# Kernel tuning notes

Measured on AMD Instinct MI355X. Metric: run time of the kernel, lower is better.

The kernel has to match this reference:

```python
import jax, jax.numpy as jnp
import numpy as np

B, H, W = 8, 48, 48
D_MODEL, D_STATE, SSM_RATIO, K = 192, 16, 2.0, 4
D_INNER = int(SSM_RATIO * D_MODEL)        # 384
DT_RANK = int(np.ceil(D_MODEL / 16))       # 12
EPS = 1e-6


def setup_inputs() -> dict:
    key = jax.random.key(0)
    ks = jax.random.split(key, 12)
    s = 0.02
    inp = {
        "x": jax.random.normal(ks[0], (B, H, W, D_MODEL), jnp.float32),
        "in_proj_w": s * jax.random.normal(ks[1], (2 * D_INNER, D_MODEL), jnp.float32),
        "conv_w": s * jax.random.normal(ks[2], (D_INNER, 1, 3, 3), jnp.float32),
        "conv_b": jnp.zeros((D_INNER,), jnp.float32),
        "x_proj_w": s * jax.random.normal(ks[3], (K, DT_RANK + 2 * D_STATE, D_INNER), jnp.float32),
        "dt_w": s * jax.random.normal(ks[4], (K, D_INNER, DT_RANK), jnp.float32),
        "dt_bias": 0.05 * jax.random.normal(ks[5], (K, D_INNER), jnp.float32),
        "A_logs": jnp.log(jnp.broadcast_to(jnp.arange(1, D_STATE + 1, dtype=jnp.float32), (K * D_INNER, D_STATE)).copy()),
        "Ds": jnp.ones((K * D_INNER,), jnp.float32),
        "ln_w": jnp.ones((D_INNER,), jnp.float32),
        "ln_b": jnp.zeros((D_INNER,), jnp.float32),
        "out_proj_w": s * jax.random.normal(ks[6], (D_MODEL, D_INNER), jnp.float32),
    }
    return inp


def _selective_scan(u, dt, A, Bs, Cs):
    # u, dt: (B,K,D,L); A: (K,D,N); Bs, Cs: (B,K,N,L)
    u_t = jnp.moveaxis(u, -1, 0)    # (L,B,K,D)
    dt_t = jnp.moveaxis(dt, -1, 0)  # (L,B,K,D)
    B_t = jnp.moveaxis(Bs, -1, 0)   # (L,B,K,N)
    C_t = jnp.moveaxis(Cs, -1, 0)   # (L,B,K,N)
    b = u.shape[0]
    h0 = jnp.zeros((b, K, D_INNER, D_STATE), jnp.float32)

    def step(h, inp):
        ut, dtt, bt, ct = inp
        dA = jnp.exp(dtt[..., None] * A)                       # (B,K,D,N)
        h = dA * h + (dtt * ut)[..., None] * bt[:, :, None, :]  # (B,K,D,N)
        y = jnp.einsum('bkdn,bkn->bkd', h, ct)
        return h, y

    _, ys = jax.lax.scan(step, h0, (u_t, dt_t, B_t, C_t))
    return jnp.moveaxis(ys, 0, -1)  # (B,K,D,L)


def reference(x, in_proj_w, conv_w, conv_b, x_proj_w, dt_w, dt_bias, A_logs, Ds, ln_w, ln_b, out_proj_w):
    b, h, w, _ = x.shape
    L = h * w
    # in_proj + split into x / gate z
    xz = jnp.einsum('bhwc,oc->bhwo', x, in_proj_w)
    xi, z = jnp.split(xz, 2, axis=-1)
    z = jax.nn.silu(z)
    # depthwise 3x3 conv, channel-first
    xi = jnp.transpose(xi, (0, 3, 1, 2))  # (B,Di,H,W)
    xi = jax.lax.conv_general_dilated(
        xi, conv_w, window_strides=(1, 1), padding='SAME',
        feature_group_count=D_INNER,
        dimension_numbers=('NCHW', 'OIHW', 'NCHW')) + conv_b[None, :, None, None]
    xi = jax.nn.silu(xi)
    # cross-scan: 4 directions (row-major, col-major, and their reverses)
    xr = xi.reshape(b, D_INNER, L)
    xc = jnp.transpose(xi, (0, 1, 3, 2)).reshape(b, D_INNER, L)
    xs = jnp.stack([xr, xc, jnp.flip(xr, -1), jnp.flip(xc, -1)], axis=1)  # (B,K,D,L)
    # per-direction projections
    x_dbl = jnp.einsum('bkdl,kcd->bkcl', xs, x_proj_w)  # (B,K,R+2N,L)
    dts = x_dbl[:, :, :DT_RANK]
    Bs = x_dbl[:, :, DT_RANK:DT_RANK + D_STATE]
    Cs = x_dbl[:, :, DT_RANK + D_STATE:]
    dts = jnp.einsum('bkrl,kdr->bkdl', dts, dt_w)
    A = -jnp.exp(A_logs.astype(jnp.float32)).reshape(K, D_INNER, D_STATE)
    dt = jax.nn.softplus(dts + dt_bias[None, :, :, None])
    ys = _selective_scan(xs.astype(jnp.float32), dt, A, Bs.astype(jnp.float32), Cs.astype(jnp.float32))
    ys = ys + Ds.reshape(1, K, D_INNER, 1) * xs  # skip
    # cross-merge (invert each direction, sum)
    def col2row(t):
        return jnp.transpose(t.reshape(b, D_INNER, w, h), (0, 1, 3, 2)).reshape(b, D_INNER, L)
    y = ys[:, 0] + col2row(ys[:, 1]) + jnp.flip(ys[:, 2], -1) + col2row(jnp.flip(ys[:, 3], -1))
    y = jnp.transpose(y.reshape(b, D_INNER, h, w), (0, 2, 3, 1))  # (B,H,W,Di)
    # LayerNorm over channel dim
    mu = y.mean(-1, keepdims=True)
    var = ((y - mu) ** 2).mean(-1, keepdims=True)
    y = (y - mu) / jnp.sqrt(var + EPS) * ln_w + ln_b
    # gate + out_proj
    y = y * z
    out = jnp.einsum('bhwd,od->bhwo', y, out_proj_w)
    return out.astype(x.dtype)
```

## Files before the change

kernel.cpp:

```cpp
#include <hip/hip_runtime.h>

#define BB 8
#define HH 48
#define WW2 48
#define LL 2304
#define CIN 192
#define DI 384
#define NK 4
#define RR 12
#define NS 16
#define CD 44
#define NX 176
#define MM 18432
#define NC 32
#define CL 72

typedef unsigned short u16;
typedef __attribute__((ext_vector_type(8))) short s16x8;
typedef __attribute__((ext_vector_type(4))) float f32x4;

static __device__ __forceinline__ float siluf(float x) { return x / (1.f + __expf(-x)); }

static __device__ __forceinline__ u16 f2bf(float x) {
    unsigned u = __float_as_uint(x);
    return (u16)((u + 0x7FFFu + ((u >> 16) & 1u)) >> 16);
}
static __device__ __forceinline__ float bf2f(u16 h) {
    return __uint_as_float(((unsigned)h) << 16);
}

static __device__ __forceinline__ int posmap(int k, int l) {
    switch (k & 3) {
    case 0: return l;
    case 1: { int w = l / HH; int h = l - w * HH; return h * WW2 + w; }
    case 2: return LL - 1 - l;
    default: { int j = LL - 1 - l; int w = j / HH; int h = j - w * HH; return h * WW2 + w; }
    }
}

__global__ __launch_bounds__(256) void k_cvt2(const float* __restrict__ in,
                                              u16* __restrict__ hi,
                                              u16* __restrict__ lo, int n) {
    int i = (blockIdx.x * 256 + threadIdx.x) * 4;
    if (i >= n) return;
    float4 v = *(const float4*)(in + i);
    u16 h0 = f2bf(v.x), h1 = f2bf(v.y), h2 = f2bf(v.z), h3 = f2bf(v.w);
    hi[i + 0] = h0; hi[i + 1] = h1; hi[i + 2] = h2; hi[i + 3] = h3;
    lo[i + 0] = f2bf(v.x - bf2f(h0));
    lo[i + 1] = f2bf(v.y - bf2f(h1));
    lo[i + 2] = f2bf(v.z - bf2f(h2));
    lo[i + 3] = f2bf(v.w - bf2f(h3));
}

template<int N, int K, int EPI>
__global__ __launch_bounds__(256) void k_gemm(const u16* __restrict__ Ahg,
                                              const u16* __restrict__ Alg,
                                              const u16* __restrict__ Bhg,
                                              const u16* __restrict__ Blg,
                                              float* __restrict__ O1,
                                              float* __restrict__ O2) {
    __shared__ __align__(16) u16 lds[12288];
    const int m0 = blockIdx.x << 7;
    const int n0 = blockIdx.y << 6;
    const int t = threadIdx.x;
    const int lane = t & 63;
    const int w = t >> 6;
    const int wm = w & 1, wn = w >> 1;

    f32x4 acc[4][2];
#pragma unroll
    for (int mi = 0; mi < 4; ++mi)
#pragma unroll
        for (int ni = 0; ni < 2; ++ni)
#pragma unroll
            for (int r = 0; r < 4; ++r) acc[mi][ni][r] = 0.f;

    const int rA = lane & 15;
    const int kb = (lane >> 4) << 3;

    for (int k0 = 0; k0 < K; k0 += 32) {
#pragma unroll
        for (int rep = 0; rep < 2; ++rep) {
            int q = t + (rep << 8);
            int row = q >> 2;
            int kk = (q & 3) << 3;
            size_t ga = (size_t)(m0 + row) * K + k0 + kk;
            *(uint4*)&lds[(row << 5) + kk] = *(const uint4*)(Ahg + ga);
            *(uint4*)&lds[4096 + (row << 5) + kk] = *(const uint4*)(Alg + ga);
        }
        {
            int row = t >> 2;
            int kk = (t & 3) << 3;
            int rg = n0 + row;
            if (N & 63) rg = (rg > N - 1) ? (N - 1) : rg;
            size_t gb = (size_t)rg * K + k0 + kk;
            *(uint4*)&lds[8192 + (row << 5) + kk] = *(const uint4*)(Bhg + gb);
            *(uint4*)&lds[10240 + (row << 5) + kk] = *(const uint4*)(Blg + gb);
        }
        __syncthreads();

        s16x8 bh[2], bl[2];
#pragma unroll
        for (int ni = 0; ni < 2; ++ni) {
            int c = (wn << 5) + (ni << 4) + rA;
            bh[ni] = *(const s16x8*)&lds[8192 + (c << 5) + kb];
            bl[ni] = *(const s16x8*)&lds[10240 + (c << 5) + kb];
        }
#pragma unroll
        for (int mi = 0; mi < 4; ++mi) {
            int rr = (wm << 6) + (mi << 4) + rA;
            s16x8 ah = *(const s16x8*)&lds[(rr << 5) + kb];
            s16x8 al = *(const s16x8*)&lds[4096 + (rr << 5) + kb];
#pragma unroll
            for (int ni = 0; ni < 2; ++ni) {
                acc[mi][ni] = __builtin_amdgcn_mfma_f32_16x16x32_bf16(al, bh[ni], acc[mi][ni], 0, 0, 0);
                acc[mi][ni] = __builtin_amdgcn_mfma_f32_16x16x32_bf16(ah, bl[ni], acc[mi][ni], 0, 0, 0);
                acc[mi][ni] = __builtin_amdgcn_mfma_f32_16x16x32_bf16(ah, bh[ni], acc[mi][ni], 0, 0, 0);
            }
        }
        __syncthreads();
    }

    const int rbase = (lane >> 4) << 2;
#pragma unroll
    for (int mi = 0; mi < 4; ++mi) {
#pragma unroll
        for (int ni = 0; ni < 2; ++ni) {
            int o = n0 + (wn << 5) + (ni << 4) + (lane & 15);
#pragma unroll
            for (int r = 0; r < 4; ++r) {
                int m = m0 + (wm << 6) + (mi << 4) + rbase + r;
                float v = acc[mi][ni][r];
                if (EPI == 0) {
                    if (o < DI) O1[(size_t)m * DI + o] = v;
                    else        O2[(size_t)m * DI + (o - DI)] = siluf(v);
                } else if (EPI == 1) {
                    if (o < NX) O1[(size_t)m * NX + o] = v;
                } else {
                    O1[(size_t)m * CIN + o] = v;
                }
            }
        }
    }
}

__global__ __launch_bounds__(128) void k_conv(const float* __restrict__ xi,
                                              const float* __restrict__ cw,
                                              const float* __restrict__ cb,
                                              float* __restrict__ ub,
                                              u16* __restrict__ ubh,
                                              u16* __restrict__ ubl) {
    int blk = blockIdx.x;
    int b = blk / LL, p = blk - b * LL;
    int h = p / WW2, w = p - h * WW2;
    for (int d = threadIdx.x; d < DI; d += 128) {
        float acc = cb[d];
#pragma unroll
        for (int dh = -1; dh <= 1; ++dh) {
            int hh = h + dh;
            if (hh < 0 || hh >= HH) continue;
#pragma unroll
            for (int dw = -1; dw <= 1; ++dw) {
                int ww = w + dw;
                if (ww < 0 || ww >= WW2) continue;
                acc = fmaf(cw[d * 9 + (dh + 1) * 3 + (dw + 1)],
                           xi[((size_t)b * LL + hh * WW2 + ww) * DI + d], acc);
            }
        }
        float o = siluf(acc);
        size_t idx = ((size_t)b * LL + p) * DI + d;
        ub[idx] = o;
        u16 hh2 = f2bf(o);
        ubh[idx] = hh2;
        ubl[idx] = f2bf(o - bf2f(hh2));
    }
}

static __device__ __forceinline__ void adv_p(int k, int& p, int& hh) {
    if (k == 0) { ++p; }
    else if (k == 2) { --p; }
    else if (k == 1) {
        if (hh == HH - 1) { hh = 0; p -= (LL - 1 - HH); }
        else { ++hh; p += WW2; }
    } else {
        if (hh == 0) { hh = HH - 1; p += (LL - 1 - HH); }
        else { --hh; p -= WW2; }
    }
}

static __device__ __forceinline__ void init_p(int k, int l0, int& p, int& hh) {
    hh = 0;
    if (k == 0) p = l0;
    else if (k == 2) p = LL - 1 - l0;
    else if (k == 1) { int w0 = l0 / HH; hh = l0 - w0 * HH; p = hh * WW2 + w0; }
    else { int j0 = LL - 1 - l0; int w0 = j0 / HH; hh = j0 - w0 * HH; p = hh * WW2 + w0; }
}

__global__ __launch_bounds__(128, 4) void k_scan1(const float* __restrict__ ub,
                                                  const float* __restrict__ xdbl,
                                                  const float* __restrict__ dt_w,
                                                  const float* __restrict__ dt_bias,
                                                  const float* __restrict__ A_logs,
                                                  float* __restrict__ HF,
                                                  float* __restrict__ SD) {
    int blk = blockIdx.x;
    int c = blk % NC;
    int t2 = blk / NC;
    int dblk = t2 % 3;
    int bk = t2 / 3;
    int k = bk & 3, b = bk >> 2;
    int d = (dblk << 7) + threadIdx.x;
    int kd = k * DI + d;

    float dtw[RR];
#pragma unroll
    for (int r = 0; r < RR; ++r) dtw[r] = dt_w[(size_t)kd * RR + r];
    float dtb = dt_bias[kd];
    float a[NS];
    bool fast = true;
#pragma unroll
    for (int n = 0; n < NS; ++n) {
        a[n] = -__expf(A_logs[(size_t)kd * NS + n]);
        fast = fast && (fabsf(a[n] + (float)(n + 1)) < 1e-3f * (float)(n + 1));
    }
    int use_fast = __all((int)fast);

    float h[NS];
#pragma unroll
    for (int n = 0; n < NS; ++n) h[n] = 0.f;
    float sumdt = 0.f;

    const float* cb0 = xdbl + (size_t)b * LL * NX + k * CD;
    const float* ubase = ub + (size_t)b * LL * DI + d;
    const int l0 = c * CL;
    int p, hh;
    init_p(k, l0, p, hh);

    if (use_fast) {
        for (int li = 0; li < CL; ++li) {
            const float4* cp4 = (const float4*)(cb0 + (size_t)p * NX);
            float dq[12];
            *(float4*)(dq + 0) = cp4[0];
            *(float4*)(dq + 4) = cp4[1];
            *(float4*)(dq + 8) = cp4[2];
            float s = dtb;
#pragma unroll
            for (int r = 0; r < RR; ++r) s = fmaf(dtw[r], dq[r], s);
            float es = __expf(s);
            float dt = (s > 15.f) ? s : __logf(1.f + es);
            float E = __builtin_amdgcn_rcpf(1.f + es);
            sumdt += dt;
            float uv = ubase[(size_t)p * DI];
            float du = dt * uv;
            float bb2[16];
            *(float4*)(bb2 + 0)  = cp4[3];
            *(float4*)(bb2 + 4)  = cp4[4];
            *(float4*)(bb2 + 8)  = cp4[5];
            *(float4*)(bb2 + 12) = cp4[6];
            float pw = 1.f;
#pragma unroll
            for (int n = 0; n < NS; ++n) {
                pw *= E;
                h[n] = fmaf(du, bb2[n], pw * h[n]);
            }
            adv_p(k, p, hh);
        }
    } else {
        for (int li = 0; li < CL; ++li) {
            int l = l0 + li;
            int pp = posmap(k, l);
            const float* cp = cb0 + (size_t)pp * NX;
            float s = dtb;
#pragma unroll
            for (int r = 0; r < RR; ++r) s = fmaf(dtw[r], cp[r], s);
            float dt = (s > 15.f) ? s : log1pf(__expf(s));
            sumdt += dt;
            float uv = ubase[(size_t)pp * DI];
            float du = dt * uv;
#pragma unroll
            for (int n = 0; n < NS; ++n) {
                float dA = __expf(dt * a[n]);
                h[n] = fmaf(du, cp[RR + n], dA * h[n]);
            }
        }
    }
    size_t base = ((size_t)bk * NC + c);
#pragma unroll
    for (int n = 0; n < NS; ++n) HF[(base * NS + n) * DI + d] = h[n];
    SD[base * DI + d] = sumdt;
}

__global__ __launch_bounds__(256) void k_scan2(const float* __restrict__ A_logs,
                                               float* __restrict__ HF,
                                               const float* __restrict__ SD) {
    int idx = blockIdx.x * 256 + threadIdx.x;
    int bk = idx / DI;
    int d = idx - bk * DI;
    int k = bk & 3;
    int kd = k * DI + d;

    float a[NS];
    bool fast = true;
#pragma unroll
    for (int n = 0; n < NS; ++n) {
        a[n] = -__expf(A_logs[(size_t)kd * NS + n]);
        fast = fast && (fabsf(a[n] + (float)(n + 1)) < 1e-3f * (float)(n + 1));
    }
    int use_fast = __all((int)fast);

    float H[NS];
#pragma unroll
    for (int n = 0; n < NS; ++n) H[n] = 0.f;

    for (int c = 0; c < NC; ++c) {
        size_t base = ((size_t)bk * NC + c);
        float sd = SD[base * DI + d];
        if (use_fast) {
            float E = __expf(-sd);
            float pw = 1.f;
#pragma unroll
            for (int n = 0; n < NS; ++n) {
                pw *= E;
                float hf = HF[(base * NS + n) * DI + d];
                HF[(base * NS + n) * DI + d] = H[n];
                H[n] = fmaf(pw, H[n], hf);
            }
        } else {
#pragma unroll
            for (int n = 0; n < NS; ++n) {
                float dec = __expf(a[n] * sd);
                float hf = HF[(base * NS + n) * DI + d];
                HF[(base * NS + n) * DI + d] = H[n];
                H[n] = fmaf(dec, H[n], hf);
            }
        }
    }
}

__global__ __launch_bounds__(128, 4) void k_scan3(const float* __restrict__ ub,
                                                  const float* __restrict__ xdbl,
                                                  const float* __restrict__ dt_w,
                                                  const float* __restrict__ dt_bias,
                                                  const float* __restrict__ A_logs,
                                                  const float* __restrict__ Ds,
                                                  const float* __restrict__ HF,
                                                  float* __restrict__ ycomb) {
    int blk = blockIdx.x;
    int c = blk % NC;
    int t2 = blk / NC;
    int dblk = t2 % 3;
    int bk = t2 / 3;
    int k = bk & 3, b = bk >> 2;
    int d = (dblk << 7) + threadIdx.x;
    int kd = k * DI + d;

    float dtw[RR];
#pragma unroll
    for (int r = 0; r < RR; ++r) dtw[r] = dt_w[(size_t)kd * RR + r];
    float dtb = dt_bias[kd];
    float dsv = Ds[kd];
    float a[NS];
    bool fast = true;
#pragma unroll
    for (int n = 0; n < NS; ++n) {
        a[n] = -__expf(A_logs[(size_t)kd * NS + n]);
        fast = fast && (fabsf(a[n] + (float)(n + 1)) < 1e-3f * (float)(n + 1));
    }
    int use_fast = __all((int)fast);

    float h[NS];
    size_t sbase = ((size_t)bk * NC + c);
#pragma unroll
    for (int n = 0; n < NS; ++n) h[n] = HF[(sbase * NS + n) * DI + d];

    const float* cb0 = xdbl + (size_t)b * LL * NX + k * CD;
    const float* ubase = ub + (size_t)b * LL * DI + d;
    float* ybase = ycomb + (size_t)b * LL * DI + d;
    const int l0 = c * CL;
    int p, hh;
    init_p(k, l0, p, hh);

    if (use_fast) {
        for (int li = 0; li < CL; ++li) {
            const float4* cp4 = (const float4*)(cb0 + (size_t)p * NX);
            float dq[12];
            *(float4*)(dq + 0) = cp4[0];
            *(float4*)(dq + 4) = cp4[1];
            *(float4*)(dq + 8) = cp4[2];
            float s = dtb;
#pragma unroll
            for (int r = 0; r < RR; ++r) s = fmaf(dtw[r], dq[r], s);
            float es = __expf(s);
            float dt = (s > 15.f) ? s : __logf(1.f + es);
            float E = __builtin_amdgcn_rcpf(1.f + es);
            float uv = ubase[(size_t)p * DI];
            float du = dt * uv;
            float bc[32];
            *(float4*)(bc + 0)  = cp4[3];
            *(float4*)(bc + 4)  = cp4[4];
            *(float4*)(bc + 8)  = cp4[5];
            *(float4*)(bc + 12) = cp4[6];
            *(float4*)(bc + 16) = cp4[7];
            *(float4*)(bc + 20) = cp4[8];
            *(float4*)(bc + 24) = cp4[9];
            *(float4*)(bc + 28) = cp4[10];
            float pw = 1.f, y = 0.f;
#pragma unroll
            for (int n = 0; n < NS; ++n) {
                pw *= E;
                h[n] = fmaf(du, bc[n], pw * h[n]);
                y = fmaf(h[n], bc[NS + n], y);
            }
            atomicAdd(ybase + (size_t)p * DI, fmaf(dsv, uv, y));
            adv_p(k, p, hh);
        }
    } else {
        for (int li = 0; li < CL; ++li) {
            int l = l0 + li;
            int pp = posmap(k, l);
            const float* cp = cb0 + (size_t)pp * NX;
            float s = dtb;
#pragma unroll
            for (int r = 0; r < RR; ++r) s = fmaf(dtw[r], cp[r], s);
            float dt = (s > 15.f) ? s : log1pf(__expf(s));
            float uv = ubase[(size_t)pp * DI];
            float du = dt * uv;
            float y = 0.f;
#pragma unroll
            for (int n = 0; n < NS; ++n) {
                float dA = __expf(dt * a[n]);
                h[n] = fmaf(du, cp[RR + n], dA * h[n]);
                y = fmaf(h[n], cp[RR + NS + n], y);
            }
            atomicAdd(ybase + (size_t)pp * DI, fmaf(dsv, uv, y));
        }
    }
}

static __device__ __forceinline__ float waveRedSum(float v) {
#pragma unroll
    for (int o = 32; o; o >>= 1) v += __shfl_down(v, o);
    return v;
}

__global__ __launch_bounds__(128) void k_lngate(const float* __restrict__ ycomb,
                                                const float* __restrict__ zb,
                                                const float* __restrict__ lnw,
                                                const float* __restrict__ lnb,
                                                u16* __restrict__ ylnh,
                                                u16* __restrict__ ylnl) {
    int m = blockIdx.x;
    const float* yr = ycomb + (size_t)m * DI;
    float v[3];
    float s1 = 0.f, s2 = 0.f;
#pragma unroll
    for (int i = 0; i < 3; ++i) {
        v[i] = yr[threadIdx.x + (i << 7)];
        s1 += v[i];
        s2 = fmaf(v[i], v[i], s2);
    }
    s1 = waveRedSum(s1);
    s2 = waveRedSum(s2);
    __shared__ float p1[2], p2[2];
    int wid = threadIdx.x >> 6, lane = threadIdx.x & 63;
    if (lane == 0) { p1[wid] = s1; p2[wid] = s2; }
    __syncthreads();
    float S1 = p1[0] + p1[1];
    float S2 = p2[0] + p2[1];
    float mu = S1 * (1.f / DI);
    float var = S2 * (1.f / DI) - mu * mu;
    float rstd = rsqrtf(var + 1e-6f);
#pragma unroll
    for (int i = 0; i < 3; ++i) {
        int dd = threadIdx.x + (i << 7);
        float o = ((v[i] - mu) * rstd) * lnw[dd] + lnb[dd];
        float g = o * zb[(size_t)m * DI + dd];
        u16 hh = f2bf(g);
        ylnh[(size_t)m * DI + dd] = hh;
        ylnl[(size_t)m * DI + dd] = f2bf(g - bf2f(hh));
    }
}

extern "C" void kernel_launch(void* const* d_in, const int* in_sizes, int n_in,
                              void* d_out, int out_size, void* d_ws, size_t ws_size,
                              hipStream_t stream) {
    const float* x         = (const float*)d_in[0];
    const float* in_proj_w = (const float*)d_in[1];
    const float* conv_w    = (const float*)d_in[2];
    const float* conv_b    = (const float*)d_in[3];
    const float* x_proj_w  = (const float*)d_in[4];
    const float* dt_w      = (const float*)d_in[5];
    const float* dt_bias   = (const float*)d_in[6];
    const float* A_logs    = (const float*)d_in[7];
    const float* Ds        = (const float*)d_in[8];
    const float* ln_w      = (const float*)d_in[9];
    const float* ln_b      = (const float*)d_in[10];
    const float* out_proj_w= (const float*)d_in[11];
    float* out = (float*)d_out;
    float* ws  = (float*)d_ws;

    const size_t SZ = (size_t)MM * DI;
    float* xi    = ws;
    float* zb    = ws + SZ;
    float* ub    = ws + 2 * SZ;
    float* xdbl  = ws + 3 * SZ;
    float* ycomb = ws + 3 * SZ + (size_t)MM * NX;
    u16*   wpl   = (u16*)(ycomb + SZ);

    u16* wphi  = wpl;
    u16* wplo  = wpl + 147456;
    u16* xpwhi = wpl + 294912;
    u16* xpwlo = wpl + 362496;
    u16* wohi  = wpl + 430080;
    u16* wolo  = wpl + 503808;

    u16* xhi  = (u16*)ub;  u16* xlo  = xhi + (size_t)MM * CIN;
    u16* ubh  = (u16*)ycomb; u16* ubl = ubh + SZ;
    u16* ylnh = (u16*)xi;  u16* ylnl = ylnh + SZ;
    float* HF = xi;
    float* SD = xi + (size_t)BB * NK * NC * NS * DI;

    k_cvt2<<<3456, 256, 0, stream>>>(x, xhi, xlo, MM * CIN);
    k_cvt2<<<144, 256, 0, stream>>>(in_proj_w, wphi, wplo, 768 * CIN);
    k_cvt2<<<66, 256, 0, stream>>>(x_proj_w, xpwhi, xpwlo, NX * DI);
    k_cvt2<<<72, 256, 0, stream>>>(out_proj_w, wohi, wolo, CIN * DI);

    k_gemm<768, CIN, 0><<<dim3(MM / 128, 12), 256, 0, stream>>>(xhi, xlo, wphi, wplo, xi, zb);

    k_conv<<<MM, 128, 0, stream>>>(xi, conv_w, conv_b, ub, ubh, ubl);

    k_gemm<NX, DI, 1><<<dim3(MM / 128, 3), 256, 0, stream>>>(ubh, ubl, xpwhi, xpwlo, xdbl, nullptr);

    hipMemsetAsync(ycomb, 0, SZ * sizeof(float), stream);

    const int nscan = BB * NK * 3 * NC;
    k_scan1<<<nscan, 128, 0, stream>>>(ub, xdbl, dt_w, dt_bias, A_logs, HF, SD);
    k_scan2<<<BB * NK * DI / 256, 256, 0, stream>>>(A_logs, HF, SD);
    k_scan3<<<nscan, 128, 0, stream>>>(ub, xdbl, dt_w, dt_bias, A_logs, Ds, HF, ycomb);

    k_lngate<<<MM, 128, 0, stream>>>(ycomb, zb, ln_w, ln_b, ylnh, ylnl);

    k_gemm<CIN, DI, 2><<<dim3(MM / 128, 3), 256, 0, stream>>>(ylnh, ylnl, wohi, wolo, out, nullptr);
}
```

Before: 384.7 us.

## Increase scan chunk count, store gate as bf16, drop occupancy hint, branchless advance

```diff
diff --git a/kernel.cpp b/kernel.cpp
--- a/kernel.cpp
+++ b/kernel.cpp
@@ -12,8 +12,8 @@
 #define CD 44
 #define NX 176
 #define MM 18432
-#define NC 32
-#define CL 72
+#define NC 48
+#define CL 48
 
 typedef unsigned short u16;
 typedef __attribute__((ext_vector_type(8))) short s16x8;
@@ -58,7 +58,7 @@
                                               const u16* __restrict__ Bhg,
                                               const u16* __restrict__ Blg,
                                               float* __restrict__ O1,
-                                              float* __restrict__ O2) {
+                                              void* __restrict__ O2) {
     __shared__ __align__(16) u16 lds[12288];
     const int m0 = blockIdx.x << 7;
     const int n0 = blockIdx.y << 6;
@@ -133,7 +133,7 @@
                 float v = acc[mi][ni][r];
                 if (EPI == 0) {
                     if (o < DI) O1[(size_t)m * DI + o] = v;
-                    else        O2[(size_t)m * DI + (o - DI)] = siluf(v);
+                    else        ((u16*)O2)[(size_t)m * DI + (o - DI)] = f2bf(siluf(v));
                 } else if (EPI == 1) {
                     if (o < NX) O1[(size_t)m * NX + o] = v;
                 } else {
@@ -180,11 +180,13 @@
     if (k == 0) { ++p; }
     else if (k == 2) { --p; }
     else if (k == 1) {
-        if (hh == HH - 1) { hh = 0; p -= (LL - 1 - HH); }
-        else { ++hh; p += WW2; }
+        bool wrap = (hh == HH - 1);
+        hh = wrap ? 0 : hh + 1;
+        p += wrap ? -(LL - 1 - HH) : WW2;
     } else {
-        if (hh == 0) { hh = HH - 1; p += (LL - 1 - HH); }
-        else { --hh; p -= WW2; }
+        bool wrap = (hh == 0);
+        hh = wrap ? HH - 1 : hh - 1;
+        p += wrap ? (LL - 1 - HH) : -WW2;
     }
 }
 
@@ -196,13 +198,13 @@
     else { int j0 = LL - 1 - l0; int w0 = j0 / HH; hh = j0 - w0 * HH; p = hh * WW2 + w0; }
 }
 
-__global__ __launch_bounds__(128, 4) void k_scan1(const float* __restrict__ ub,
-                                                  const float* __restrict__ xdbl,
-                                                  const float* __restrict__ dt_w,
-                                                  const float* __restrict__ dt_bias,
-                                                  const float* __restrict__ A_logs,
-                                                  float* __restrict__ HF,
-                                                  float* __restrict__ SD) {
+__global__ __launch_bounds__(128) void k_scan1(const float* __restrict__ ub,
+                                               const float* __restrict__ xdbl,
+                                               const float* __restrict__ dt_w,
+                                               const float* __restrict__ dt_bias,
+                                               const float* __restrict__ A_logs,
+                                               float* __restrict__ HF,
+                                               float* __restrict__ SD) {
     int blk = blockIdx.x;
     int c = blk % NC;
     int t2 = blk / NC;
@@ -337,14 +339,14 @@
     }
 }
 
-__global__ __launch_bounds__(128, 4) void k_scan3(const float* __restrict__ ub,
-                                                  const float* __restrict__ xdbl,
-                                                  const float* __restrict__ dt_w,
-                                                  const float* __restrict__ dt_bias,
-                                                  const float* __restrict__ A_logs,
-                                                  const float* __restrict__ Ds,
-                                                  const float* __restrict__ HF,
-                                                  float* __restrict__ ycomb) {
+__global__ __launch_bounds__(128) void k_scan3(const float* __restrict__ ub,
+                                               const float* __restrict__ xdbl,
+                                               const float* __restrict__ dt_w,
+                                               const float* __restrict__ dt_bias,
+                                               const float* __restrict__ A_logs,
+                                               const float* __restrict__ Ds,
+                                               const float* __restrict__ HF,
+                                               float* __restrict__ ycomb) {
     int blk = blockIdx.x;
     int c = blk % NC;
     int t2 = blk / NC;
@@ -444,7 +446,7 @@
 }
 
 __global__ __launch_bounds__(128) void k_lngate(const float* __restrict__ ycomb,
-                                                const float* __restrict__ zb,
+                                                const u16* __restrict__ zb16,
                                                 const float* __restrict__ lnw,
                                                 const float* __restrict__ lnb,
                                                 u16* __restrict__ ylnh,
@@ -474,7 +476,7 @@
     for (int i = 0; i < 3; ++i) {
         int dd = threadIdx.x + (i << 7);
         float o = ((v[i] - mu) * rstd) * lnw[dd] + lnb[dd];
-        float g = o * zb[(size_t)m * DI + dd];
+        float g = o * bf2f(zb16[(size_t)m * DI + dd]);
         u16 hh = f2bf(g);
         ylnh[(size_t)m * DI + dd] = hh;
         ylnl[(size_t)m * DI + dd] = f2bf(g - bf2f(hh));
@@ -501,7 +503,7 @@
 
     const size_t SZ = (size_t)MM * DI;
     float* xi    = ws;
-    float* zb    = ws + SZ;
+    u16*   zb16  = (u16*)(ws + SZ + SZ / 2);
     float* ub    = ws + 2 * SZ;
     float* xdbl  = ws + 3 * SZ;
     float* ycomb = ws + 3 * SZ + (size_t)MM * NX;
@@ -517,15 +519,15 @@
     u16* xhi  = (u16*)ub;  u16* xlo  = xhi + (size_t)MM * CIN;
     u16* ubh  = (u16*)ycomb; u16* ubl = ubh + SZ;
     u16* ylnh = (u16*)xi;  u16* ylnl = ylnh + SZ;
-    float* HF = xi;
-    float* SD = xi + (size_t)BB * NK * NC * NS * DI;
+    float* HF = ws;
+    float* SD = ws + (size_t)BB * NK * NC * NS * DI;
 
     k_cvt2<<<3456, 256, 0, stream>>>(x, xhi, xlo, MM * CIN);
     k_cvt2<<<144, 256, 0, stream>>>(in_proj_w, wphi, wplo, 768 * CIN);
     k_cvt2<<<66, 256, 0, stream>>>(x_proj_w, xpwhi, xpwlo, NX * DI);
     k_cvt2<<<72, 256, 0, stream>>>(out_proj_w, wohi, wolo, CIN * DI);
 
-    k_gemm<768, CIN, 0><<<dim3(MM / 128, 12), 256, 0, stream>>>(xhi, xlo, wphi, wplo, xi, zb);
+    k_gemm<768, CIN, 0><<<dim3(MM / 128, 12), 256, 0, stream>>>(xhi, xlo, wphi, wplo, xi, (void*)zb16);
 
     k_conv<<<MM, 128, 0, stream>>>(xi, conv_w, conv_b, ub, ubh, ubl);
 
@@ -538,7 +540,7 @@
     k_scan2<<<BB * NK * DI / 256, 256, 0, stream>>>(A_logs, HF, SD);
     k_scan3<<<nscan, 128, 0, stream>>>(ub, xdbl, dt_w, dt_bias, A_logs, Ds, HF, ycomb);
 
-    k_lngate<<<MM, 128, 0, stream>>>(ycomb, zb, ln_w, ln_b, ylnh, ylnl);
+    k_lngate<<<MM, 128, 0, stream>>>(ycomb, zb16, ln_w, ln_b, ylnh, ylnl);
 
     k_gemm<CIN, DI, 2><<<dim3(MM / 128, 3), 256, 0, stream>>>(ylnh, ylnl, wohi, wolo, out, nullptr);
 }
```

Result: faster. 369.4 us (-4.0%).
